# Optimization experiments

Hardware: AMD Instinct MI355X
Metric: run time of the kernel (lower is better)

The kernel has to match this reference:

```python
import jax, jax.numpy as jnp
import numpy as np

B, S, D_IN, H, D_HEAD = 4, 1024, 768, 12, 64


def setup_inputs() -> dict:
    key = jax.random.key(0)
    k1, k2, k3, k4 = jax.random.split(key, 4)
    x = jax.random.normal(k1, (B, S, D_IN), dtype=jnp.float32)
    # Per-head projection weights stored as [H, d_in, d_head] (equivalent to
    # nn.Linear weight [d_head, d_in] applied as x @ W.T), scaled like default init.
    scale = 1.0 / np.sqrt(D_IN)
    Wq = jax.random.normal(k2, (H, D_IN, D_HEAD), dtype=jnp.float32) * scale
    Wk = jax.random.normal(k3, (H, D_IN, D_HEAD), dtype=jnp.float32) * scale
    Wv = jax.random.normal(k4, (H, D_IN, D_HEAD), dtype=jnp.float32) * scale
    return {"x": x, "Wq": Wq, "Wk": Wk, "Wv": Wv}


def reference(x, Wq, Wk, Wv):
    # Vectorized over heads; faithful to per-head causal attention then concat.
    q = jnp.einsum("bsd,hde->bhse", x, Wq)  # [B,H,S,Dh]
    k = jnp.einsum("bsd,hde->bhse", x, Wk)
    v = jnp.einsum("bsd,hde->bhse", x, Wv)
    scale = 1.0 / jnp.sqrt(jnp.asarray(D_HEAD, dtype=q.dtype))
    scores = jnp.einsum("bhse,bhte->bhst", q, k) * scale  # [B,H,S,S]
    causal = jnp.tril(jnp.ones((S, S), dtype=bool))
    scores = jnp.where(causal, scores, jnp.finfo(scores.dtype).min)
    attn = jax.nn.softmax(scores, axis=-1)  # dropout p=0.0 (eval) -> identity
    ctx = jnp.einsum("bhst,bhte->bhse", attn, v)  # [B,H,S,Dh]
    # concat heads along last dim: [B,S,H*Dh]
    return jnp.transpose(ctx, (0, 2, 1, 3)).reshape(B, S, H * D_HEAD)
```

## Files before the change

kernel.cpp:

```cpp
#include <hip/hip_runtime.h>
#include <hip/hip_bf16.h>

#define NB 4
#define SS 1024
#define DIN 768
#define NH 12
#define DH 64

typedef float f32x4 __attribute__((ext_vector_type(4)));
typedef short bf16x8 __attribute__((ext_vector_type(8)));

static __device__ __forceinline__ unsigned short f2bf(float f) {
    __hip_bfloat16 h = __float2bfloat16(f);
    return *reinterpret_cast<unsigned short*>(&h);
}

static __device__ __forceinline__ float exp2_fast(float x) {
    return __builtin_amdgcn_exp2f(x);
}

static __device__ __forceinline__ void gload16(const void* g, void* l) {
    __builtin_amdgcn_global_load_lds(
        (const __attribute__((address_space(1))) void*)g,
        (__attribute__((address_space(3))) void*)l, 16, 0, 0);
}

__global__ void cast_x_kernel(const float* __restrict__ x, unsigned short* __restrict__ xb) {
    int i = (blockIdx.x * 256 + threadIdx.x) * 4;
    float4 v = *reinterpret_cast<const float4*>(x + i);
    ushort4 o;
    o.x = f2bf(v.x); o.y = f2bf(v.y); o.z = f2bf(v.z); o.w = f2bf(v.w);
    *reinterpret_cast<ushort4*>(xb + i) = o;
}

__global__ void transpose_w_kernel(const float* __restrict__ Wq, const float* __restrict__ Wk,
                                   const float* __restrict__ Wv, unsigned short* __restrict__ wt) {
    __shared__ float lds[64][68];
    int d0 = blockIdx.x * 64;
    int h  = blockIdx.y;
    int p  = blockIdx.z;
    const float* W = (p == 0) ? Wq : (p == 1) ? Wk : Wv;
    const float* base = W + (size_t)h * DIN * DH;
    int tid = threadIdx.x;
    int rr = tid >> 4, c4 = tid & 15;
#pragma unroll
    for (int i = 0; i < 4; ++i) {
        int d = i * 16 + rr;
        float4 v = *reinterpret_cast<const float4*>(base + (size_t)(d0 + d) * DH + c4 * 4);
        lds[d][c4 * 4 + 0] = v.x; lds[d][c4 * 4 + 1] = v.y;
        lds[d][c4 * 4 + 2] = v.z; lds[d][c4 * 4 + 3] = v.w;
    }
    __syncthreads();
    unsigned short* outp = wt + ((size_t)(p * NH + h) * DH) * DIN;
#pragma unroll
    for (int i = 0; i < 4; ++i) {
        int e = i * 16 + rr;
        int dc = c4 * 4;
        ushort4 o;
        o.x = f2bf(lds[dc + 0][e]); o.y = f2bf(lds[dc + 1][e]);
        o.z = f2bf(lds[dc + 2][e]); o.w = f2bf(lds[dc + 3][e]);
        *reinterpret_cast<ushort4*>(outp + (size_t)e * DIN + d0 + dc) = o;
    }
}

__global__ __launch_bounds__(256) void qkv_gemm_kernel(
    const unsigned short* __restrict__ xb, const unsigned short* __restrict__ wt,
    unsigned short* __restrict__ qb, unsigned short* __restrict__ kb,
    unsigned short* __restrict__ vT) {
    __shared__ __align__(16) unsigned char smem[28672];
    unsigned short* a_lds = (unsigned short*)smem;
    unsigned short* b_lds = (unsigned short*)(smem + 16384);

    int m0 = blockIdx.x * 128;
    int n0 = blockIdx.y * 96;
    int tid = threadIdx.x, lane = tid & 63, w = tid >> 6;
    int l15 = lane & 15, hi4 = (lane >> 4) * 4, hi8 = (lane >> 4) * 8;
    int wr = w >> 1, wc = w & 1;
    int srow = tid >> 3;
    int scolb = (tid & 7) * 16;
    int sw = (l15 & 7) << 4;

    f32x4 acc[4][3] = {};

    for (int k0 = 0; k0 < DIN; k0 += 64) {
        __syncthreads();
#pragma unroll
        for (int i = 0; i < 4; ++i) {
            int row = i * 32 + srow;
            int cb = scolb ^ ((row & 7) << 4);
            gload16(xb + (size_t)(m0 + row) * DIN + k0 + (cb >> 1), a_lds + row * 64 + (scolb >> 1));
        }
#pragma unroll
        for (int i = 0; i < 3; ++i) {
            int row = i * 32 + srow;
            int cb = scolb ^ ((row & 7) << 4);
            gload16(wt + (size_t)(n0 + row) * DIN + k0 + (cb >> 1), b_lds + row * 64 + (scolb >> 1));
        }
        __syncthreads();
#pragma unroll
        for (int kk = 0; kk < 64; kk += 32) {
            int cb = ((kk + hi8) * 2) ^ sw;
            bf16x8 af[4], bfr[3];
#pragma unroll
            for (int m = 0; m < 4; ++m)
                af[m] = *reinterpret_cast<const bf16x8*>(a_lds + (wr * 64 + m * 16 + l15) * 64 + (cb >> 1));
#pragma unroll
            for (int n = 0; n < 3; ++n)
                bfr[n] = *reinterpret_cast<const bf16x8*>(b_lds + (wc * 48 + n * 16 + l15) * 64 + (cb >> 1));
#pragma unroll
            for (int m = 0; m < 4; ++m)
#pragma unroll
                for (int n = 0; n < 3; ++n)
                    acc[m][n] = __builtin_amdgcn_mfma_f32_16x16x32_bf16(af[m], bfr[n], acc[m][n], 0, 0, 0);
        }
    }
    __syncthreads();

    int p  = n0 / 768;
    int cp = (n0 % 768) + wc * 48;
    int b  = m0 >> 10;
    int s_base = (m0 & 1023) + wr * 64;

    if (p < 2) {
        float qs = (p == 0) ? 0.180336880f : 1.0f;
        unsigned short* dstb = (p == 0) ? qb : kb;
#pragma unroll
        for (int m = 0; m < 4; ++m)
#pragma unroll
            for (int n = 0; n < 3; ++n)
#pragma unroll
                for (int r = 0; r < 4; ++r) {
                    int col = cp + n * 16 + l15;
                    int h = col >> 6, e = col & 63;
                    dstb[((size_t)(b * NH + h) * SS + s_base + m * 16 + hi4 + r) * DH + e] =
                        f2bf(acc[m][n][r] * qs);
                }
    } else {
        float* sc = (float*)smem + w * 784;
#pragma unroll
        for (int m = 0; m < 4; ++m) {
#pragma unroll
            for (int n = 0; n < 3; ++n)
#pragma unroll
                for (int r = 0; r < 4; ++r)
                    sc[(hi4 + r) * 49 + n * 16 + l15] = acc[m][n][r];
            if (lane < 48) {
                unsigned short vv[16];
#pragma unroll
                for (int t = 0; t < 16; ++t) vv[t] = f2bf(sc[t * 49 + lane]);
                int col = cp + lane;
                int h = col >> 6, e = col & 63;
                unsigned short* dst = vT + ((size_t)(b * NH + h) * DH + e) * SS + s_base + m * 16;
                *reinterpret_cast<uint4*>(dst)     = *reinterpret_cast<const uint4*>(vv);
                *reinterpret_cast<uint4*>(dst + 8) = *reinterpret_cast<const uint4*>(vv + 8);
            }
        }
    }
}

struct AttnCtx {
    const unsigned short* kg;
    const unsigned short* vg;
    char* smem;
    unsigned short* pw;
    int srow, scolb, l15, hi, sw;
};

static __device__ __forceinline__ void attn_stage(const AttnCtx& c, int buf, int kv) {
    unsigned short* kl = (unsigned short*)(c.smem + buf * 8192);
    unsigned short* vl = (unsigned short*)(c.smem + 16384 + buf * 8192);
#pragma unroll
    for (int i = 0; i < 2; ++i) {
        int row = i * 32 + c.srow;
        int cb = c.scolb ^ ((row & 7) << 4);
        gload16(c.kg + (size_t)(kv * 64 + row) * DH + (cb >> 1), kl + row * 64 + (c.scolb >> 1));
        gload16(c.vg + (size_t)row * SS + kv * 64 + (cb >> 1),   vl + row * 64 + (c.scolb >> 1));
    }
}

template<bool DIAG>
static __device__ __forceinline__ void attn_step(
    const AttnCtx& c, int buf, int kv, int qg,
    bf16x8 qf0, bf16x8 qf1, float& m_r, float& l_r, f32x4 o_acc[4]) {
    const unsigned short* kl = (const unsigned short*)(c.smem + buf * 8192);
    const unsigned short* vl = (const unsigned short*)(c.smem + 16384 + buf * 8192);
    int l15 = c.l15, hi = c.hi, sw = c.sw;
    int hi4 = hi * 4, hi8 = hi * 8;

    f32x4 sacc[4] = {};
    __builtin_amdgcn_s_setprio(1);
#pragma unroll
    for (int s = 0; s < 2; ++s) {
        int cb = ((32 * s + hi8) * 2) ^ sw;
#pragma unroll
        for (int n = 0; n < 4; ++n) {
            bf16x8 kf = *reinterpret_cast<const bf16x8*>(kl + (16 * n + l15) * 64 + (cb >> 1));
            sacc[n] = __builtin_amdgcn_mfma_f32_16x16x32_bf16(kf, s == 0 ? qf0 : qf1, sacc[n], 0, 0, 0);
        }
    }
    __builtin_amdgcn_s_setprio(0);

    float pv[4][4];
#pragma unroll
    for (int n = 0; n < 4; ++n)
#pragma unroll
        for (int r = 0; r < 4; ++r) {
            float sv = sacc[n][r];
            if (DIAG && (kv * 64 + 16 * n + hi4 + r) > qg) sv = -INFINITY;
            pv[n][r] = sv;
        }

    float mn[4];
#pragma unroll
    for (int n = 0; n < 4; ++n)
        mn[n] = fmaxf(fmaxf(pv[n][0], pv[n][1]), fmaxf(pv[n][2], pv[n][3]));
    float mx = fmaxf(fmaxf(mn[0], mn[1]), fmaxf(mn[2], mn[3]));
    mx = fmaxf(mx, __shfl_xor(mx, 16));
    mx = fmaxf(mx, __shfl_xor(mx, 32));

    if (!__all(mx - m_r <= 8.0f)) {
        float m_new = fmaxf(m_r, mx);
        float alpha = exp2_fast(m_r - m_new);
        l_r *= alpha;
#pragma unroll
        for (int n = 0; n < 4; ++n)
#pragma unroll
            for (int r = 0; r < 4; ++r) o_acc[n][r] *= alpha;
        m_r = m_new;
    }
    float sn[4];
#pragma unroll
    for (int n = 0; n < 4; ++n) {
#pragma unroll
        for (int r = 0; r < 4; ++r) pv[n][r] = exp2_fast(pv[n][r] - m_r);
        sn[n] = (pv[n][0] + pv[n][1]) + (pv[n][2] + pv[n][3]);
    }
    float sum = (sn[0] + sn[1]) + (sn[2] + sn[3]);
    sum += __shfl_xor(sum, 16);
    sum += __shfl_xor(sum, 32);
    l_r += sum;

    unsigned int* pwu = (unsigned int*)c.pw;
#pragma unroll
    for (int n = 0; n < 4; ++n)
#pragma unroll
        for (int p2 = 0; p2 < 2; ++p2) {
            unsigned int w32 = (unsigned int)f2bf(pv[n][2 * p2]) |
                               ((unsigned int)f2bf(pv[n][2 * p2 + 1]) << 16);
            pwu[l15 * 36 + 8 * n + 2 * hi + p2] = w32;
        }
    bf16x8 pa0 = *reinterpret_cast<const bf16x8*>(c.pw + l15 * 72 + hi8);
    bf16x8 pa1 = *reinterpret_cast<const bf16x8*>(c.pw + l15 * 72 + 32 + hi8);

    __builtin_amdgcn_s_setprio(1);
#pragma unroll
    for (int s = 0; s < 2; ++s) {
        int cb = ((32 * s + hi8) * 2) ^ sw;
#pragma unroll
        for (int n = 0; n < 4; ++n) {
            bf16x8 vf = *reinterpret_cast<const bf16x8*>(vl + (16 * n + l15) * 64 + (cb >> 1));
            o_acc[n] = __builtin_amdgcn_mfma_f32_16x16x32_bf16(vf, s == 0 ? pa0 : pa1, o_acc[n], 0, 0, 0);
        }
    }
    __builtin_amdgcn_s_setprio(0);
}

__global__ __launch_bounds__(256) void attn_kernel(
    const unsigned short* __restrict__ qb, const unsigned short* __restrict__ kb,
    const unsigned short* __restrict__ vT, float* __restrict__ out) {
    __shared__ __align__(16) char smem[41984];

    int bid = blockIdx.x;
    int qi = 15 - bid / 48;
    int rem = bid % 48;
    int h = rem % 12, b = rem / 12;
    int q0 = qi * 64;
    int tid = threadIdx.x, lane = tid & 63, w = tid >> 6;
    int l15 = lane & 15, hi = lane >> 4;
    size_t bh = (size_t)(b * NH + h);

    AttnCtx c;
    c.kg = kb + bh * SS * DH;
    c.vg = vT + bh * DH * SS;
    c.smem = smem;
    c.pw = (unsigned short*)(smem + 32768) + w * 1152;
    c.srow = tid >> 3; c.scolb = (tid & 7) * 16;
    c.l15 = l15; c.hi = hi; c.sw = (l15 & 7) << 4;

    int qg = q0 + 16 * w + l15;
    const unsigned short* qp = qb + (bh * SS + qg) * DH;
    bf16x8 qf0 = *reinterpret_cast<const bf16x8*>(qp + hi * 8);
    bf16x8 qf1 = *reinterpret_cast<const bf16x8*>(qp + 32 + hi * 8);

    float m_r = -INFINITY, l_r = 0.f;
    f32x4 o_acc[4] = {};

    attn_stage(c, 0, 0);
    __syncthreads();
    for (int kv = 0; kv < qi; ++kv) {
        attn_stage(c, (kv & 1) ^ 1, kv + 1);
        attn_step<false>(c, kv & 1, kv, qg, qf0, qf1, m_r, l_r, o_acc);
        __syncthreads();
    }
    attn_step<true>(c, qi & 1, qi, qg, qf0, qf1, m_r, l_r, o_acc);
    __syncthreads();

    float inv = 1.f / l_r;
    float* sc = (float*)(smem + w * 4352);
#pragma unroll
    for (int n = 0; n < 4; ++n)
#pragma unroll
        for (int r = 0; r < 4; ++r)
            sc[l15 * 68 + 16 * n + hi * 4 + r] = o_acc[n][r] * inv;
    __builtin_amdgcn_s_waitcnt(0);
#pragma unroll
    for (int j = 0; j < 4; ++j) {
        f32x4 v = *reinterpret_cast<const f32x4*>(sc + l15 * 68 + j * 16 + hi * 4);
        *reinterpret_cast<f32x4*>(out + ((size_t)b * SS + q0 + 16 * w + l15) * (NH * DH)
                                  + h * DH + j * 16 + hi * 4) = v;
    }
}

extern "C" void kernel_launch(void* const* d_in, const int* in_sizes, int n_in,
                              void* d_out, int out_size, void* d_ws, size_t ws_size,
                              hipStream_t stream) {
    const float* x  = (const float*)d_in[0];
    const float* Wq = (const float*)d_in[1];
    const float* Wk = (const float*)d_in[2];
    const float* Wv = (const float*)d_in[3];
    float* out = (float*)d_out;

    char* ws = (char*)d_ws;
    unsigned short* xb = (unsigned short*)ws;
    unsigned short* wt = (unsigned short*)(ws +  6291456);
    unsigned short* qb = (unsigned short*)(ws +  9830400);
    unsigned short* kb = (unsigned short*)(ws + 16121856);
    unsigned short* vT = (unsigned short*)(ws + 22413312);

    hipLaunchKernelGGL(cast_x_kernel,      dim3(3072),      dim3(256), 0, stream, x, xb);
    hipLaunchKernelGGL(transpose_w_kernel, dim3(12, 12, 3), dim3(256), 0, stream, Wq, Wk, Wv, wt);
    hipLaunchKernelGGL(qkv_gemm_kernel,    dim3(32, 24),    dim3(256), 0, stream, xb, wt, qb, kb, vT);
    hipLaunchKernelGGL(attn_kernel,        dim3(768),       dim3(256), 0, stream, qb, kb, vT, out);
}
```

Measured before the change: 118.8 us.

## Merge prep kernels, remap GEMM blocks, swizzle P buffer, set attention occupancy

Merges the x cast and weight transpose kernels into one prep kernel, which removes a launch and its boundary gap. Remaps the QKV GEMM to a 1D grid whose block order is permuted across the eight XCDs for better cache locality. In attention, the padded P staging buffer becomes an XOR-swizzled unpadded layout, which cuts LDS use and should avoid bank conflicts. Launch bounds now request 4 blocks per CU, which limits registers and could cause spills.

```diff
diff --git a/kernel.cpp b/kernel.cpp
--- a/kernel.cpp
+++ b/kernel.cpp
@@ -25,41 +25,41 @@
         (__attribute__((address_space(3))) void*)l, 16, 0, 0);
 }
 
-__global__ void cast_x_kernel(const float* __restrict__ x, unsigned short* __restrict__ xb) {
-    int i = (blockIdx.x * 256 + threadIdx.x) * 4;
-    float4 v = *reinterpret_cast<const float4*>(x + i);
-    ushort4 o;
-    o.x = f2bf(v.x); o.y = f2bf(v.y); o.z = f2bf(v.z); o.w = f2bf(v.w);
-    *reinterpret_cast<ushort4*>(xb + i) = o;
-}
-
-__global__ void transpose_w_kernel(const float* __restrict__ Wq, const float* __restrict__ Wk,
-                                   const float* __restrict__ Wv, unsigned short* __restrict__ wt) {
+__global__ void prep_kernel(const float* __restrict__ x, const float* __restrict__ Wq,
+                            const float* __restrict__ Wk, const float* __restrict__ Wv,
+                            unsigned short* __restrict__ xb, unsigned short* __restrict__ wt) {
     __shared__ float lds[64][68];
-    int d0 = blockIdx.x * 64;
-    int h  = blockIdx.y;
-    int p  = blockIdx.z;
-    const float* W = (p == 0) ? Wq : (p == 1) ? Wk : Wv;
-    const float* base = W + (size_t)h * DIN * DH;
-    int tid = threadIdx.x;
-    int rr = tid >> 4, c4 = tid & 15;
-#pragma unroll
-    for (int i = 0; i < 4; ++i) {
-        int d = i * 16 + rr;
-        float4 v = *reinterpret_cast<const float4*>(base + (size_t)(d0 + d) * DH + c4 * 4);
-        lds[d][c4 * 4 + 0] = v.x; lds[d][c4 * 4 + 1] = v.y;
-        lds[d][c4 * 4 + 2] = v.z; lds[d][c4 * 4 + 3] = v.w;
-    }
-    __syncthreads();
-    unsigned short* outp = wt + ((size_t)(p * NH + h) * DH) * DIN;
-#pragma unroll
-    for (int i = 0; i < 4; ++i) {
-        int e = i * 16 + rr;
-        int dc = c4 * 4;
+    int bid = blockIdx.x, tid = threadIdx.x;
+    {
+        int i = (bid * 256 + tid) * 4;
+        float4 v = *reinterpret_cast<const float4*>(x + i);
         ushort4 o;
-        o.x = f2bf(lds[dc + 0][e]); o.y = f2bf(lds[dc + 1][e]);
-        o.z = f2bf(lds[dc + 2][e]); o.w = f2bf(lds[dc + 3][e]);
-        *reinterpret_cast<ushort4*>(outp + (size_t)e * DIN + d0 + dc) = o;
+        o.x = f2bf(v.x); o.y = f2bf(v.y); o.z = f2bf(v.z); o.w = f2bf(v.w);
+        *reinterpret_cast<ushort4*>(xb + i) = o;
+    }
+    if (bid < 432) {
+        int d0 = (bid % 12) * 64, h = (bid / 12) % 12, p = bid / 144;
+        const float* W = (p == 0) ? Wq : (p == 1) ? Wk : Wv;
+        const float* base = W + (size_t)h * DIN * DH;
+        int rr = tid >> 4, c4 = tid & 15;
+#pragma unroll
+        for (int i = 0; i < 4; ++i) {
+            int d = i * 16 + rr;
+            float4 v = *reinterpret_cast<const float4*>(base + (size_t)(d0 + d) * DH + c4 * 4);
+            lds[d][c4 * 4 + 0] = v.x; lds[d][c4 * 4 + 1] = v.y;
+            lds[d][c4 * 4 + 2] = v.z; lds[d][c4 * 4 + 3] = v.w;
+        }
+        __syncthreads();
+        unsigned short* outp = wt + ((size_t)(p * NH + h) * DH) * DIN;
+#pragma unroll
+        for (int i = 0; i < 4; ++i) {
+            int e = i * 16 + rr;
+            int dc = c4 * 4;
+            ushort4 o;
+            o.x = f2bf(lds[dc + 0][e]); o.y = f2bf(lds[dc + 1][e]);
+            o.z = f2bf(lds[dc + 2][e]); o.w = f2bf(lds[dc + 3][e]);
+            *reinterpret_cast<ushort4*>(outp + (size_t)e * DIN + d0 + dc) = o;
+        }
     }
 }
 
@@ -71,8 +71,9 @@
     unsigned short* a_lds = (unsigned short*)smem;
     unsigned short* b_lds = (unsigned short*)(smem + 16384);
 
-    int m0 = blockIdx.x * 128;
-    int n0 = blockIdx.y * 96;
+    int sb = (blockIdx.x & 7) * 96 + (blockIdx.x >> 3);
+    int m0 = (sb & 31) * 128;
+    int n0 = (sb >> 5) * 96;
     int tid = threadIdx.x, lane = tid & 63, w = tid >> 6;
     int l15 = lane & 15, hi4 = (lane >> 4) * 4, hi8 = (lane >> 4) * 8;
     int wr = w >> 1, wc = w & 1;
@@ -147,7 +148,7 @@
             if (lane < 48) {
                 unsigned short vv[16];
 #pragma unroll
-                for (int t = 0; t < 16; ++t) vv[t] = f2bf(sc[t * 49 + lane]);
+                for (int t2 = 0; t2 < 16; ++t2) vv[t2] = f2bf(sc[t2 * 49 + lane]);
                 int col = cp + lane;
                 int h = col >> 6, e = col & 63;
                 unsigned short* dst = vT + ((size_t)(b * NH + h) * DH + e) * SS + s_base + m * 16;
@@ -240,6 +241,7 @@
     sum += __shfl_xor(sum, 32);
     l_r += sum;
 
+    int xr = (l15 & 7) * 4;
     unsigned int* pwu = (unsigned int*)c.pw;
 #pragma unroll
     for (int n = 0; n < 4; ++n)
@@ -247,10 +249,12 @@
         for (int p2 = 0; p2 < 2; ++p2) {
             unsigned int w32 = (unsigned int)f2bf(pv[n][2 * p2]) |
                                ((unsigned int)f2bf(pv[n][2 * p2 + 1]) << 16);
-            pwu[l15 * 36 + 8 * n + 2 * hi + p2] = w32;
-        }
-    bf16x8 pa0 = *reinterpret_cast<const bf16x8*>(c.pw + l15 * 72 + hi8);
-    bf16x8 pa1 = *reinterpret_cast<const bf16x8*>(c.pw + l15 * 72 + 32 + hi8);
+            pwu[l15 * 32 + ((8 * n + 2 * hi + p2) ^ xr)] = w32;
+        }
+    int i0 = (4 * hi) ^ xr;
+    int i1 = (16 + 4 * hi) ^ xr;
+    bf16x8 pa0 = *reinterpret_cast<const bf16x8*>(c.pw + l15 * 64 + i0 * 2);
+    bf16x8 pa1 = *reinterpret_cast<const bf16x8*>(c.pw + l15 * 64 + i1 * 2);
 
     __builtin_amdgcn_s_setprio(1);
 #pragma unroll
@@ -265,10 +269,10 @@
     __builtin_amdgcn_s_setprio(0);
 }
 
-__global__ __launch_bounds__(256) void attn_kernel(
+__global__ __launch_bounds__(256, 4) void attn_kernel(
     const unsigned short* __restrict__ qb, const unsigned short* __restrict__ kb,
     const unsigned short* __restrict__ vT, float* __restrict__ out) {
-    __shared__ __align__(16) char smem[41984];
+    __shared__ __align__(16) char smem[40960];
 
     int bid = blockIdx.x;
     int qi = 15 - bid / 48;
@@ -277,20 +281,21 @@
     int q0 = qi * 64;
     int tid = threadIdx.x, lane = tid & 63, w = tid >> 6;
     int l15 = lane & 15, hi = lane >> 4;
+    int hi4 = hi * 4, hi8 = hi * 8;
     size_t bh = (size_t)(b * NH + h);
 
     AttnCtx c;
     c.kg = kb + bh * SS * DH;
     c.vg = vT + bh * DH * SS;
     c.smem = smem;
-    c.pw = (unsigned short*)(smem + 32768) + w * 1152;
+    c.pw = (unsigned short*)(smem + 32768) + w * 1024;
     c.srow = tid >> 3; c.scolb = (tid & 7) * 16;
     c.l15 = l15; c.hi = hi; c.sw = (l15 & 7) << 4;
 
     int qg = q0 + 16 * w + l15;
     const unsigned short* qp = qb + (bh * SS + qg) * DH;
-    bf16x8 qf0 = *reinterpret_cast<const bf16x8*>(qp + hi * 8);
-    bf16x8 qf1 = *reinterpret_cast<const bf16x8*>(qp + 32 + hi * 8);
+    bf16x8 qf0 = *reinterpret_cast<const bf16x8*>(qp + hi8);
+    bf16x8 qf1 = *reinterpret_cast<const bf16x8*>(qp + 32 + hi8);
 
     float m_r = -INFINITY, l_r = 0.f;
     f32x4 o_acc[4] = {};
@@ -311,13 +316,13 @@
     for (int n = 0; n < 4; ++n)
 #pragma unroll
         for (int r = 0; r < 4; ++r)
-            sc[l15 * 68 + 16 * n + hi * 4 + r] = o_acc[n][r] * inv;
+            sc[l15 * 68 + 16 * n + hi4 + r] = o_acc[n][r] * inv;
     __builtin_amdgcn_s_waitcnt(0);
 #pragma unroll
     for (int j = 0; j < 4; ++j) {
-        f32x4 v = *reinterpret_cast<const f32x4*>(sc + l15 * 68 + j * 16 + hi * 4);
+        f32x4 v = *reinterpret_cast<const f32x4*>(sc + l15 * 68 + j * 16 + hi4);
         *reinterpret_cast<f32x4*>(out + ((size_t)b * SS + q0 + 16 * w + l15) * (NH * DH)
-                                  + h * DH + j * 16 + hi * 4) = v;
+                                  + h * DH + j * 16 + hi4) = v;
     }
 }
 
@@ -337,8 +342,7 @@
     unsigned short* kb = (unsigned short*)(ws + 16121856);
     unsigned short* vT = (unsigned short*)(ws + 22413312);
 
-    hipLaunchKernelGGL(cast_x_kernel,      dim3(3072),      dim3(256), 0, stream, x, xb);
-    hipLaunchKernelGGL(transpose_w_kernel, dim3(12, 12, 3), dim3(256), 0, stream, Wq, Wk, Wv, wt);
-    hipLaunchKernelGGL(qkv_gemm_kernel,    dim3(32, 24),    dim3(256), 0, stream, xb, wt, qb, kb, vT);
-    hipLaunchKernelGGL(attn_kernel,        dim3(768),       dim3(256), 0, stream, qb, kb, vT, out);
-}
+    hipLaunchKernelGGL(prep_kernel,     dim3(3072), dim3(256), 0, stream, x, Wq, Wk, Wv, xb, wt);
+    hipLaunchKernelGGL(qkv_gemm_kernel, dim3(768),  dim3(256), 0, stream, xb, wt, qb, kb, vT);
+    hipLaunchKernelGGL(attn_kernel,     dim3(768),  dim3(256), 0, stream, qb, kb, vT, out);
+}
```

New measurement: 116.2 us. 1.02x faster.
